# Performance work log

Measured on AMD Instinct MI355X. Metric: run time of the kernel, lower is better.

Reference implementation:

```python
import jax, jax.numpy as jnp
import numpy as np

C, B, N, D, H, DV = 8, 32, 256, 128, 4, 64  # channels, graphs, nodes/graph, gcn_h_dim, heads, d_kv
EPS = 1e-6


def _layernorm(x, g, b):
    mu = jnp.mean(x, axis=-1, keepdims=True)
    var = jnp.mean(jnp.square(x - mu), axis=-1, keepdims=True)
    return (x - mu) * jax.lax.rsqrt(var + EPS) * g + b


def setup_inputs() -> dict:
    key = jax.random.key(0)
    ks = jax.random.split(key, 6)
    gnn_out = jax.random.normal(ks[0], (C, B * N, D), dtype=jnp.float32)
    batch = jnp.repeat(jnp.arange(B, dtype=jnp.int64), N)  # sorted node->graph ids
    s = 0.05  # small init scale keeps softmax well-conditioned
    Wq = jax.random.normal(ks[1], (D, H * DV), dtype=jnp.float32) * s
    Wk = jax.random.normal(ks[2], (D, H * DV), dtype=jnp.float32) * s
    Wv = jax.random.normal(ks[3], (D, H * DV), dtype=jnp.float32) * s
    Wfc = jax.random.normal(ks[4], (H * DV, DV), dtype=jnp.float32) * s
    return {
        "gnn_out": gnn_out,
        "Wq": Wq, "Wk": Wk, "Wv": Wv, "Wfc": Wfc,
        "ln1_g": jnp.ones((DV,), jnp.float32), "ln1_b": jnp.zeros((DV,), jnp.float32),
        "ln2_g": jnp.ones((DV,), jnp.float32), "ln2_b": jnp.zeros((DV,), jnp.float32),
        "batch": batch,
        "sz_b": B,
    }


def reference(gnn_out, Wq, Wk, Wv, Wfc, ln1_g, ln1_b, ln2_g, ln2_b, batch, sz_b):
    sz_c, total, d_model = gnn_out.shape
    nb = sz_b                      # static number of graphs
    n = total // nb                # nodes per graph (equal-sized graphs)
    dv = Wfc.shape[1]
    nh = Wq.shape[1] // dv

    # to_dense_batch for all channels at once: scatter nodes into [B, N, C, D]
    starts = jnp.searchsorted(batch, jnp.arange(nb))
    pos = jnp.arange(total) - starts[batch]
    dense = jnp.zeros((nb, n, sz_c, d_model), gnn_out.dtype)
    dense = dense.at[batch, pos].set(jnp.transpose(gnn_out, (1, 0, 2)))
    x = jnp.transpose(dense, (2, 0, 1, 3)).reshape(sz_c * nb, n, d_model)  # fold channel into batch

    # multi-head projections -> [CB, H, N, dv]
    q = (x @ Wq).reshape(sz_c * nb, n, nh, dv).transpose(0, 2, 1, 3)
    k = (x @ Wk).reshape(sz_c * nb, n, nh, dv).transpose(0, 2, 1, 3)
    v = (x @ Wv).reshape(sz_c * nb, n, nh, dv).transpose(0, 2, 1, 3)

    temp = dv ** 0.5
    attn = jax.nn.softmax(jnp.einsum('bhqd,bhkd->bhqk', q / temp, k), axis=-1)
    # non-standard: out = V^T @ attn @ V  -> [CB, H, dv, dv]
    out = jnp.einsum('bhnd,bhnm->bhdm', v, attn)
    out = jnp.einsum('bhdm,bhme->bhde', out, v)

    out = out.transpose(0, 2, 1, 3).reshape(sz_c * nb, dv, nh * dv)  # [CB, dv, H*dv]
    out = _layernorm(out @ Wfc, ln1_g, ln1_b)                        # [CB, dv, dv]

    out = out.reshape(sz_c, nb, dv, dv).transpose(1, 0, 2, 3)        # [B, C, dv, dv]
    return _layernorm(out, ln2_g, ln2_b)
```

## Files before the change

### kernel.cpp

```cpp
#include <hip/hip_runtime.h>

#define NN 256
#define DM 128
#define NH 4
#define LK 72
#define LT 264

typedef __bf16 bf16;
typedef __attribute__((ext_vector_type(8))) __bf16 bf16x8;
typedef __attribute__((ext_vector_type(4))) float f32x4;
typedef __attribute__((ext_vector_type(16))) float f32x16;

static __device__ __forceinline__ unsigned short f2b(float f) {
  return __builtin_bit_cast(unsigned short, (__bf16)f);
}
static __device__ __forceinline__ bf16x8 ldf(const unsigned short* p) {
  return *(const bf16x8*)p;
}
static __device__ __forceinline__ void st4(unsigned short* p, float a, float b, float c, float d) {
  ushort4 v; v.x = f2b(a); v.y = f2b(b); v.z = f2b(c); v.w = f2b(d);
  *(ushort4*)p = v;
}

#define MFMA16(a,b,c) __builtin_amdgcn_mfma_f32_16x16x32_bf16((a),(b),(c),0,0,0)
#define MFMA32(a,b,c) __builtin_amdgcn_mfma_f32_32x32x16_bf16((a),(b),(c),0,0,0)
#define Z4  {0.f,0.f,0.f,0.f}
#define Z16 {0.f,0.f,0.f,0.f,0.f,0.f,0.f,0.f,0.f,0.f,0.f,0.f,0.f,0.f,0.f,0.f}

#define XELEMS (256u * 16u * 256u * 8u)
#define WQO 0
#define WKO 32768
#define WVO 65536
#define WFO 98304

__global__ void prep_x_kernel(const float* __restrict__ gnn, unsigned short* __restrict__ x2) {
  const int tid = blockIdx.x * 256 + threadIdx.x;
  const int cb  = tid >> 10;
  const int r   = tid & 1023;
  const int dgq = r >> 8;
  const int n   = r & 255;
  const float* src = gnn + ((size_t)cb * 256 + n) * 128;
  unsigned short* dstb = x2 + (size_t)cb * (16 * 256 * 8);
#pragma unroll
  for (int i = 0; i < 4; ++i) {
    const int dg = dgq * 4 + i;
    float4 a = *(const float4*)(src + dg * 8);
    float4 b = *(const float4*)(src + dg * 8 + 4);
    ushort4 u0, u1;
    u0.x = f2b(a.x); u0.y = f2b(a.y); u0.z = f2b(a.z); u0.w = f2b(a.w);
    u1.x = f2b(b.x); u1.y = f2b(b.y); u1.z = f2b(b.z); u1.w = f2b(b.w);
    ushort4* d = (ushort4*)(dstb + ((size_t)dg * 256 + n) * 8);
    d[0] = u0; d[1] = u1;
  }
}

__global__ void prep_w_kernel(const float* __restrict__ Wq, const float* __restrict__ Wk,
                              const float* __restrict__ Wv, const float* __restrict__ Wfc,
                              unsigned short* __restrict__ w2) {
  const int tid = blockIdx.x * 256 + threadIdx.x;
  if (tid < 12288) {
    const int wi  = tid >> 12;
    const int r   = tid & 4095;
    const int dg  = r >> 8, col = r & 255;
    const float* W = (wi == 0) ? Wq : ((wi == 1) ? Wk : Wv);
    unsigned short* d = w2 + wi * 32768 + ((size_t)dg * 256 + col) * 8;
#pragma unroll
    for (int j = 0; j < 8; ++j) d[j] = f2b(W[(size_t)(dg * 8 + j) * 256 + col]);
  } else if (tid < 14336) {
    const int r  = tid - 12288;
    const int dg = r >> 6, col = r & 63;
    unsigned short* d = w2 + WFO + ((size_t)dg * 64 + col) * 8;
#pragma unroll
    for (int j = 0; j < 8; ++j) d[j] = f2b(Wfc[(size_t)(dg * 8 + j) * 64 + col]);
  }
}

template<bool WS>
__global__ __launch_bounds__(512, 2)
void vlrgat_kernel(const float* __restrict__ gnn,
                   const float* __restrict__ Wq, const float* __restrict__ Wk,
                   const float* __restrict__ Wv, const float* __restrict__ Wfc,
                   const float* __restrict__ ln1g, const float* __restrict__ ln1b,
                   const float* __restrict__ ln2g, const float* __restrict__ ln2b,
                   const unsigned short* __restrict__ wsx,
                   const unsigned short* __restrict__ wsw,
                   float* __restrict__ out)
{
  __shared__ __align__(16) unsigned short ks [NN * LK];
  __shared__ __align__(16) unsigned short qs [NN * LK];
  __shared__ __align__(16) unsigned short vsT[64 * LT];
  __shared__ __align__(16) unsigned short U  [NN * LK];
  __shared__ __align__(16) float sums[NN];

  const int t   = threadIdx.x;
  const int w   = t >> 6;
  const int l   = t & 63;
  const int lr  = l & 15;
  const int lg  = l >> 4;
  const int l31 = l & 31;
  const int lh  = l >> 5;
  const int g   = w & 3;
  const int cb  = blockIdx.x;
  const unsigned short* const xw = WS ? (wsx + (size_t)cb * (16 * 256 * 8)) : nullptr;

  f32x16 oacc[NH];
#pragma unroll
  for (int h = 0; h < NH; ++h) oacc[h] = (f32x16)Z16;

  auto xfrag = [&](int n0, int c) -> bf16x8 {
    if constexpr (WS) {
      return ldf(xw + (((size_t)(c * 2 + lh)) * 256 + n0 + l31) * 8);
    } else {
      const float* p = gnn + ((size_t)cb * 256 + n0 + l31) * 128 + c * 16 + lh * 8;
      bf16x8 r;
#pragma unroll
      for (int j = 0; j < 8; ++j) r[j] = (bf16)p[j];
      return r;
    }
  };
  auto wfrag = [&](int wo, const float* __restrict__ W, int c, int col) -> bf16x8 {
    if constexpr (WS) {
      return ldf(wsw + wo + (((size_t)(c * 2 + lh)) * 256 + col) * 8);
    } else {
      bf16x8 r;
#pragma unroll
      for (int j = 0; j < 8; ++j) r[j] = (bf16)W[(size_t)(c * 16 + lh * 8 + j) * 256 + col];
      return r;
    }
  };
  auto wfcfrag = [&](int kt, int col) -> bf16x8 {
    if constexpr (WS) {
      return ldf(wsw + WFO + (((size_t)(kt * 4 + lg)) * 64 + col) * 8);
    } else {
      bf16x8 r;
#pragma unroll
      for (int j = 0; j < 8; ++j) r[j] = (bf16)Wfc[(size_t)(kt * 32 + lg * 8 + j) * 64 + col];
      return r;
    }
  };

#pragma unroll
  for (int h = 0; h < NH; ++h) {
    const float* const WAp = (w < 4) ? Wk : Wv;
    const int       woA    = (w < 4) ? WKO : WVO;
    bf16x8 wA[2][8], wQ[8];
#pragma unroll
    for (int e = 0; e < 2; ++e)
#pragma unroll
      for (int c = 0; c < 8; ++c)
        wA[e][c] = wfrag(woA, WAp, c, h * 64 + e * 32 + l31);
    const int qcol = h * 64 + ((w < 4) ? 0 : 32) + l31;
#pragma unroll
    for (int c = 0; c < 8; ++c)
      wQ[c] = wfrag(WQO, Wq, c, qcol);

    __syncthreads();

#pragma unroll
    for (int half = 0; half < 2; ++half) {
      const int n0 = half * 128 + g * 32;
      bf16x8 xa[8];
#pragma unroll
      for (int c = 0; c < 8; ++c) xa[c] = xfrag(n0, c);
      if (w < 4) {
#pragma unroll
        for (int e = 0; e < 2; ++e) {
          f32x16 a = Z16;
#pragma unroll
          for (int c = 0; c < 8; ++c) a = MFMA32(wA[e][c], xa[c], a);
#pragma unroll
          for (int g2 = 0; g2 < 4; ++g2)
            st4(&ks[(n0 + l31) * LK + e * 32 + g2 * 8 + lh * 4],
                a[g2*4], a[g2*4+1], a[g2*4+2], a[g2*4+3]);
        }
        f32x16 a = Z16;
#pragma unroll
        for (int c = 0; c < 8; ++c) a = MFMA32(wQ[c], xa[c], a);
#pragma unroll
        for (int g2 = 0; g2 < 4; ++g2)
          st4(&qs[(n0 + l31) * LK + g2 * 8 + lh * 4],
              a[g2*4]*0.125f, a[g2*4+1]*0.125f, a[g2*4+2]*0.125f, a[g2*4+3]*0.125f);
      } else {
#pragma unroll
        for (int e = 0; e < 2; ++e) {
          f32x16 a = Z16;
#pragma unroll
          for (int c = 0; c < 8; ++c) a = MFMA32(xa[c], wA[e][c], a);
#pragma unroll
          for (int g2 = 0; g2 < 4; ++g2)
            st4(&vsT[(e * 32 + l31) * LT + n0 + g2 * 8 + lh * 4],
                a[g2*4], a[g2*4+1], a[g2*4+2], a[g2*4+3]);
        }
        f32x16 a = Z16;
#pragma unroll
        for (int c = 0; c < 8; ++c) a = MFMA32(wQ[c], xa[c], a);
#pragma unroll
        for (int g2 = 0; g2 < 4; ++g2)
          st4(&qs[(n0 + l31) * LK + 32 + g2 * 8 + lh * 4],
              a[g2*4]*0.125f, a[g2*4+1]*0.125f, a[g2*4+2]*0.125f, a[g2*4+3]*0.125f);
      }
    }
    __syncthreads();

    bf16x8 qf[4];
#pragma unroll
    for (int kt = 0; kt < 4; ++kt)
      qf[kt] = ldf(&qs[(w * 32 + l31) * LK + kt * 16 + lh * 8]);
    unsigned short* const Pw = &U[(w * 32) * LK];
    f32x16 racc[2]; racc[0] = (f32x16)Z16; racc[1] = (f32x16)Z16;
    float psum = 0.f;
#pragma unroll
    for (int kh = 0; kh < 2; ++kh) {
      f32x16 sh[4];
#pragma unroll
      for (int mb = 0; mb < 4; ++mb) {
        sh[mb] = (f32x16)Z16;
#pragma unroll
        for (int kt = 0; kt < 4; ++kt)
          sh[mb] = MFMA32(ldf(&ks[((kh * 4 + mb) * 32 + l31) * LK + kt * 16 + lh * 8]),
                          qf[kt], sh[mb]);
      }
#pragma unroll
      for (int mb = 0; mb < 4; ++mb)
#pragma unroll
        for (int i = 0; i < 16; ++i) {
          sh[mb][i] = __expf(sh[mb][i]);
          psum += sh[mb][i];
        }
#pragma unroll
      for (int sl = 0; sl < 2; ++sl) {
#pragma unroll
        for (int mbl = 0; mbl < 2; ++mbl) {
          const f32x16& s = sh[sl * 2 + mbl];
#pragma unroll
          for (int g2 = 0; g2 < 4; ++g2)
            st4(&Pw[l31 * LK + mbl * 32 + g2 * 8 + lh * 4],
                s[g2*4], s[g2*4+1], s[g2*4+2], s[g2*4+3]);
        }
        const int kb = kh * 128 + sl * 64;
#pragma unroll
        for (int kt2 = 0; kt2 < 4; ++kt2) {
          bf16x8 pf = ldf(&Pw[l31 * LK + kt2 * 16 + lh * 8]);
          racc[0] = MFMA32(pf, ldf(&vsT[l31 * LT + kb + kt2 * 16 + lh * 8]), racc[0]);
          racc[1] = MFMA32(pf, ldf(&vsT[(32 + l31) * LT + kb + kt2 * 16 + lh * 8]), racc[1]);
        }
      }
    }
    psum += __shfl_xor(psum, 32);
    sums[w * 32 + l31] = psum;

    __syncthreads();

#pragma unroll
    for (int g2 = 0; g2 < 4; ++g2) {
      float4 sv = *(const float4*)&sums[w * 32 + g2 * 8 + lh * 4];
      const float i0 = 1.f / sv.x, i1 = 1.f / sv.y, i2 = 1.f / sv.z, i3 = 1.f / sv.w;
#pragma unroll
      for (int eb = 0; eb < 2; ++eb)
        st4(&U[(eb * 32 + l31) * LT + w * 32 + g2 * 8 + lh * 4],
            racc[eb][g2*4]*i0, racc[eb][g2*4+1]*i1, racc[eb][g2*4+2]*i2, racc[eb][g2*4+3]*i3);
    }
    __syncthreads();

    if (w < 4) {
      const int db = (w >> 1) * 32, eb = (w & 1) * 32;
#pragma unroll
      for (int kt = 0; kt < 16; ++kt)
        oacc[h] = MFMA32(ldf(&vsT[(db + l31) * LT + kt * 16 + lh * 8]),
                         ldf(&U  [(eb + l31) * LT + kt * 16 + lh * 8]), oacc[h]);
    }
  }

  __syncthreads();
  if (w < 4) {
    const int db = (w >> 1) * 32, eb = (w & 1) * 32;
#pragma unroll
    for (int h2 = 0; h2 < NH; ++h2)
#pragma unroll
      for (int g2 = 0; g2 < 4; ++g2)
#pragma unroll
        for (int r = 0; r < 4; ++r)
          U[(db + g2 * 8 + lh * 4 + r) * LT + h2 * 64 + eb + l31] = f2b(oacc[h2][g2*4+r]);
  }
  __syncthreads();

  if (w < 4) {
    bf16x8 oa[8];
#pragma unroll
    for (int kt = 0; kt < 8; ++kt)
      oa[kt] = ldf(&U[(w * 16 + lr) * LT + kt * 32 + lg * 8]);
    f32x4 fa[4];
#pragma unroll
    for (int ct = 0; ct < 4; ++ct) {
      f32x4 a = Z4;
#pragma unroll
      for (int kt = 0; kt < 8; ++kt)
        a = MFMA16(oa[kt], wfcfrag(kt, ct * 16 + lr), a);
      fa[ct] = a;
    }

    float g1v[4], b1v[4], g2v[4], b2v[4];
#pragma unroll
    for (int ct = 0; ct < 4; ++ct) {
      g1v[ct] = ln1g[ct * 16 + lr];
      b1v[ct] = ln1b[ct * 16 + lr];
      g2v[ct] = ln2g[ct * 16 + lr];
      b2v[ct] = ln2b[ct * 16 + lr];
    }
    const int bb = cb & 31;
    const int ch = cb >> 5;
    float* const obase = out + (size_t)(bb * 8 + ch) * 64 * 64;
#pragma unroll
    for (int r = 0; r < 4; ++r) {
      const int row = w * 16 + lg * 4 + r;
      float x0 = fa[0][r], x1 = fa[1][r], x2 = fa[2][r], x3 = fa[3][r];
      float mu = x0 + x1 + x2 + x3;
      mu += __shfl_xor(mu, 1); mu += __shfl_xor(mu, 2);
      mu += __shfl_xor(mu, 4); mu += __shfl_xor(mu, 8);
      mu *= 0.015625f;
      float d0 = x0 - mu, d1 = x1 - mu, d2 = x2 - mu, d3 = x3 - mu;
      float vr = d0*d0 + d1*d1 + d2*d2 + d3*d3;
      vr += __shfl_xor(vr, 1); vr += __shfl_xor(vr, 2);
      vr += __shfl_xor(vr, 4); vr += __shfl_xor(vr, 8);
      const float is1 = rsqrtf(vr * 0.015625f + 1e-6f);
      float y0 = d0*is1*g1v[0] + b1v[0];
      float y1 = d1*is1*g1v[1] + b1v[1];
      float y2 = d2*is1*g1v[2] + b1v[2];
      float y3 = d3*is1*g1v[3] + b1v[3];
      float mu2 = y0 + y1 + y2 + y3;
      mu2 += __shfl_xor(mu2, 1); mu2 += __shfl_xor(mu2, 2);
      mu2 += __shfl_xor(mu2, 4); mu2 += __shfl_xor(mu2, 8);
      mu2 *= 0.015625f;
      float e0 = y0-mu2, e1 = y1-mu2, e2 = y2-mu2, e3 = y3-mu2;
      float v2 = e0*e0 + e1*e1 + e2*e2 + e3*e3;
      v2 += __shfl_xor(v2, 1); v2 += __shfl_xor(v2, 2);
      v2 += __shfl_xor(v2, 4); v2 += __shfl_xor(v2, 8);
      const float is2 = rsqrtf(v2 * 0.015625f + 1e-6f);
      float* const op = obase + (size_t)row * 64;
      op[ 0 + lr] = e0*is2*g2v[0] + b2v[0];
      op[16 + lr] = e1*is2*g2v[1] + b2v[1];
      op[32 + lr] = e2*is2*g2v[2] + b2v[2];
      op[48 + lr] = e3*is2*g2v[3] + b2v[3];
    }
  }
}

extern "C" void kernel_launch(void* const* d_in, const int* in_sizes, int n_in,
                              void* d_out, int out_size, void* d_ws, size_t ws_size,
                              hipStream_t stream) {
  const float* gnn = (const float*)d_in[0];
  const float* Wq  = (const float*)d_in[1];
  const float* Wk  = (const float*)d_in[2];
  const float* Wv  = (const float*)d_in[3];
  const float* Wfc = (const float*)d_in[4];
  const float* l1g = (const float*)d_in[5];
  const float* l1b = (const float*)d_in[6];
  const float* l2g = (const float*)d_in[7];
  const float* l2b = (const float*)d_in[8];
  (void)in_sizes; (void)n_in; (void)out_size;

  const size_t need = ((size_t)XELEMS + 3 * 32768 + 16384) * sizeof(unsigned short);
  unsigned short* wsx = (unsigned short*)d_ws;
  unsigned short* wsw = wsx + XELEMS;

  if (d_ws != nullptr && ws_size >= need) {
    prep_x_kernel<<<dim3(1024), dim3(256), 0, stream>>>(gnn, wsx);
    prep_w_kernel<<<dim3(56), dim3(256), 0, stream>>>(Wq, Wk, Wv, Wfc, wsw);
    vlrgat_kernel<true><<<dim3(256), dim3(512), 0, stream>>>(
        gnn, Wq, Wk, Wv, Wfc, l1g, l1b, l2g, l2b, wsx, wsw, (float*)d_out);
  } else {
    vlrgat_kernel<false><<<dim3(256), dim3(512), 0, stream>>>(
        gnn, Wq, Wk, Wv, Wfc, l1g, l1b, l2g, l2b, nullptr, nullptr, (float*)d_out);
  }
}
```

Baseline: 68.76 us.

## Split attention per (channel-batch, head) into separate blocks and add FC+LayerNorm kernel

The monolithic kernel looped over all four heads in one 256-block grid. It is replaced by a head kernel that launches 1024 blocks, one per (cb, head), with smaller shared memory so four blocks fit per CU. Q now stays in registers as packed bf16 with the 1/sqrt(d) scale folded in. Each head's [64x64] output goes to a workspace buffer, and a separate kernel then does the Wfc projection and both LayerNorms. This trades an extra launch and a global round trip of the head outputs for far more parallelism on a GPU with many CUs.

Measured after the change: 98.80 us. +43.7%, slower.

```diff
diff --git a/kernel.cpp b/kernel.cpp
--- a/kernel.cpp
+++ b/kernel.cpp
@@ -10,6 +10,7 @@
 typedef __attribute__((ext_vector_type(8))) __bf16 bf16x8;
 typedef __attribute__((ext_vector_type(4))) float f32x4;
 typedef __attribute__((ext_vector_type(16))) float f32x16;
+typedef __attribute__((ext_vector_type(4))) unsigned int u32x4;
 
 static __device__ __forceinline__ unsigned short f2b(float f) {
   return __builtin_bit_cast(unsigned short, (__bf16)f);
@@ -20,6 +21,19 @@
 static __device__ __forceinline__ void st4(unsigned short* p, float a, float b, float c, float d) {
   ushort4 v; v.x = f2b(a); v.y = f2b(b); v.z = f2b(c); v.w = f2b(d);
   *(ushort4*)p = v;
+}
+static __device__ __forceinline__ unsigned cvtpk(float lo, float hi) {
+  unsigned r;
+  asm("v_cvt_pk_bf16_f32 %0, %1, %2" : "=v"(r) : "v"(lo), "v"(hi));
+  return r;
+}
+static __device__ __forceinline__ bf16x8 ld2(const unsigned short* p0, const unsigned short* p1) {
+  u32x4 t;
+  t.x = *(const unsigned*)(p0);
+  t.y = *(const unsigned*)(p0 + 2);
+  t.z = *(const unsigned*)(p1);
+  t.w = *(const unsigned*)(p1 + 2);
+  return __builtin_bit_cast(bf16x8, t);
 }
 
 #define MFMA16(a,b,c) __builtin_amdgcn_mfma_f32_16x16x32_bf16((a),(b),(c),0,0,0)
@@ -32,6 +46,8 @@
 #define WKO 32768
 #define WVO 65536
 #define WFO 98304
+#define WELEMS 114688u
+#define OELEMS (256u * 64u * 256u)
 
 __global__ void prep_x_kernel(const float* __restrict__ gnn, unsigned short* __restrict__ x2) {
   const int tid = blockIdx.x * 256 + threadIdx.x;
@@ -75,16 +91,227 @@
   }
 }
 
-template<bool WS>
+__global__ __launch_bounds__(512, 4)
+void vlrgat_head_kernel(const unsigned short* __restrict__ wsx,
+                        const unsigned short* __restrict__ wsw,
+                        unsigned short* __restrict__ wso)
+{
+  __shared__ __align__(16) unsigned short ks [NN * LK];
+  __shared__ __align__(16) unsigned short vsT[64 * LT];
+  __shared__ __align__(16) float sums[NN];
+
+  const int t   = threadIdx.x;
+  const int w   = t >> 6;
+  const int l   = t & 63;
+  const int l31 = l & 31;
+  const int lh  = l >> 5;
+  const int g   = w & 3;
+  const int bid = blockIdx.x;
+  const int cb  = bid >> 2;
+  const int h   = bid & 3;
+  const unsigned short* const xw = wsx + (size_t)cb * (16 * 256 * 8);
+
+  const int woA = (w < 4) ? WKO : WVO;
+  bf16x8 wA[2][8];
+#pragma unroll
+  for (int e = 0; e < 2; ++e)
+#pragma unroll
+    for (int c = 0; c < 8; ++c)
+      wA[e][c] = ldf(wsw + woA + (((size_t)(c * 2 + lh)) * 256 + h * 64 + e * 32 + l31) * 8);
+
+  u32x4 qu[4];
+  const int hw = w >> 2;
+#pragma unroll
+  for (int half = 0; half < 2; ++half) {
+    const int n0 = half * 128 + g * 32;
+    bf16x8 xa[8];
+#pragma unroll
+    for (int c = 0; c < 8; ++c)
+      xa[c] = ldf(xw + (((size_t)(c * 2 + lh)) * 256 + n0 + l31) * 8);
+    if (w < 4) {
+#pragma unroll
+      for (int e = 0; e < 2; ++e) {
+        f32x16 a = Z16;
+#pragma unroll
+        for (int c = 0; c < 8; ++c) a = MFMA32(wA[e][c], xa[c], a);
+#pragma unroll
+        for (int g2 = 0; g2 < 4; ++g2)
+          st4(&ks[(n0 + l31) * LK + e * 32 + g2 * 8 + lh * 4],
+              a[g2*4], a[g2*4+1], a[g2*4+2], a[g2*4+3]);
+      }
+    } else {
+#pragma unroll
+      for (int e = 0; e < 2; ++e) {
+        f32x16 a = Z16;
+#pragma unroll
+        for (int c = 0; c < 8; ++c) a = MFMA32(xa[c], wA[e][c], a);
+#pragma unroll
+        for (int g2 = 0; g2 < 4; ++g2)
+          st4(&vsT[(e * 32 + l31) * LT + n0 + g2 * 8 + lh * 4],
+              a[g2*4], a[g2*4+1], a[g2*4+2], a[g2*4+3]);
+      }
+    }
+    if (half == hw) {
+#pragma unroll
+      for (int e = 0; e < 2; ++e) {
+        bf16x8 wQ[8];
+#pragma unroll
+        for (int c = 0; c < 8; ++c)
+          wQ[c] = ldf(wsw + WQO + (((size_t)(c * 2 + lh)) * 256 + h * 64 + e * 32 + l31) * 8);
+        f32x16 a = Z16;
+#pragma unroll
+        for (int c = 0; c < 8; ++c) a = MFMA32(wQ[c], xa[c], a);
+        const float S = 0.125f;
+        qu[e*2]   = (u32x4){cvtpk(a[0]*S,  a[1]*S),  cvtpk(a[2]*S,  a[3]*S),
+                            cvtpk(a[4]*S,  a[5]*S),  cvtpk(a[6]*S,  a[7]*S)};
+        qu[e*2+1] = (u32x4){cvtpk(a[8]*S,  a[9]*S),  cvtpk(a[10]*S, a[11]*S),
+                            cvtpk(a[12]*S, a[13]*S), cvtpk(a[14]*S, a[15]*S)};
+      }
+    }
+  }
+  __syncthreads();
+
+  f32x16 racc0 = Z16, racc1 = Z16;
+  float psum = 0.f;
+  const int ko1 = 4 * lh, ko2 = 8 + 4 * lh;
+#pragma unroll
+  for (int mb = 0; mb < 8; ++mb) {
+    const unsigned short* krow = &ks[(mb * 32 + l31) * LK];
+    f32x16 s = Z16;
+#pragma unroll
+    for (int kt = 0; kt < 4; ++kt) {
+      bf16x8 kf = ld2(krow + kt * 16 + ko1, krow + kt * 16 + ko2);
+      s = MFMA32(kf, __builtin_bit_cast(bf16x8, qu[kt]), s);
+    }
+#pragma unroll
+    for (int i = 0; i < 16; ++i) { s[i] = __expf(s[i]); psum += s[i]; }
+    u32x4 pu0 = (u32x4){cvtpk(s[0], s[1]),   cvtpk(s[2], s[3]),
+                        cvtpk(s[4], s[5]),   cvtpk(s[6], s[7])};
+    u32x4 pu1 = (u32x4){cvtpk(s[8], s[9]),   cvtpk(s[10], s[11]),
+                        cvtpk(s[12], s[13]), cvtpk(s[14], s[15])};
+#pragma unroll
+    for (int b = 0; b < 2; ++b) {
+      bf16x8 pf = __builtin_bit_cast(bf16x8, b ? pu1 : pu0);
+      const unsigned short* v0 = &vsT[l31 * LT + mb * 32 + b * 16];
+      const unsigned short* v1 = &vsT[(32 + l31) * LT + mb * 32 + b * 16];
+      racc0 = MFMA32(pf, ld2(v0 + ko1, v0 + ko2), racc0);
+      racc1 = MFMA32(pf, ld2(v1 + ko1, v1 + ko2), racc1);
+    }
+  }
+  psum += __shfl_xor(psum, 32);
+  sums[w * 32 + l31] = psum;
+
+  __syncthreads();
+
+  unsigned short* const RsT = ks;
+#pragma unroll
+  for (int g2 = 0; g2 < 4; ++g2) {
+    float4 sv = *(const float4*)&sums[w * 32 + g2 * 8 + lh * 4];
+    const float i0 = 1.f / sv.x, i1 = 1.f / sv.y, i2 = 1.f / sv.z, i3 = 1.f / sv.w;
+    st4(&RsT[l31 * LT + w * 32 + g2 * 8 + lh * 4],
+        racc0[g2*4]*i0, racc0[g2*4+1]*i1, racc0[g2*4+2]*i2, racc0[g2*4+3]*i3);
+    st4(&RsT[(32 + l31) * LT + w * 32 + g2 * 8 + lh * 4],
+        racc1[g2*4]*i0, racc1[g2*4+1]*i1, racc1[g2*4+2]*i2, racc1[g2*4+3]*i3);
+  }
+  __syncthreads();
+
+  if (w < 4) {
+    const int db = (w >> 1) * 32, eb = (w & 1) * 32;
+    f32x16 o = Z16;
+#pragma unroll
+    for (int kt = 0; kt < 16; ++kt)
+      o = MFMA32(ldf(&vsT[(db + l31) * LT + kt * 16 + lh * 8]),
+                 ldf(&RsT[(eb + l31) * LT + kt * 16 + lh * 8]), o);
+    unsigned short* ob = wso + (size_t)cb * 64 * 256;
+#pragma unroll
+    for (int r = 0; r < 16; ++r) {
+      const int d = db + (r & 3) + 8 * (r >> 2) + 4 * lh;
+      ob[(size_t)d * 256 + h * 64 + eb + l31] = f2b(o[r]);
+    }
+  }
+}
+
+__global__ __launch_bounds__(256, 4)
+void fc_ln_kernel(const unsigned short* __restrict__ wso,
+                  const unsigned short* __restrict__ wsw,
+                  const float* __restrict__ ln1g, const float* __restrict__ ln1b,
+                  const float* __restrict__ ln2g, const float* __restrict__ ln2b,
+                  float* __restrict__ out)
+{
+  const int t  = threadIdx.x;
+  const int w  = t >> 6;
+  const int l  = t & 63;
+  const int lr = l & 15;
+  const int lg = l >> 4;
+  const int cb = blockIdx.x;
+  const unsigned short* ob = wso + (size_t)cb * 64 * 256;
+
+  bf16x8 oa[8];
+#pragma unroll
+  for (int kt = 0; kt < 8; ++kt)
+    oa[kt] = ldf(&ob[(w * 16 + lr) * 256 + kt * 32 + lg * 8]);
+  f32x4 fa[4];
+#pragma unroll
+  for (int ct = 0; ct < 4; ++ct) {
+    f32x4 a = Z4;
+#pragma unroll
+    for (int kt = 0; kt < 8; ++kt)
+      a = MFMA16(oa[kt], ldf(wsw + WFO + (((size_t)(kt * 4 + lg)) * 64 + ct * 16 + lr) * 8), a);
+    fa[ct] = a;
+  }
+
+  float g1v[4], b1v[4], g2v[4], b2v[4];
+#pragma unroll
+  for (int ct = 0; ct < 4; ++ct) {
+    g1v[ct] = ln1g[ct * 16 + lr];
+    b1v[ct] = ln1b[ct * 16 + lr];
+    g2v[ct] = ln2g[ct * 16 + lr];
+    b2v[ct] = ln2b[ct * 16 + lr];
+  }
+  const int bb = cb & 31;
+  const int ch = cb >> 5;
+  float* const obase = out + (size_t)(bb * 8 + ch) * 64 * 64;
+#pragma unroll
+  for (int r = 0; r < 4; ++r) {
+    const int row = w * 16 + lg * 4 + r;
+    float x0 = fa[0][r], x1 = fa[1][r], x2 = fa[2][r], x3 = fa[3][r];
+    float mu = x0 + x1 + x2 + x3;
+    mu += __shfl_xor(mu, 1); mu += __shfl_xor(mu, 2);
+    mu += __shfl_xor(mu, 4); mu += __shfl_xor(mu, 8);
+    mu *= 0.015625f;
+    float d0 = x0 - mu, d1 = x1 - mu, d2 = x2 - mu, d3 = x3 - mu;
+    float vr = d0*d0 + d1*d1 + d2*d2 + d3*d3;
+    vr += __shfl_xor(vr, 1); vr += __shfl_xor(vr, 2);
+    vr += __shfl_xor(vr, 4); vr += __shfl_xor(vr, 8);
+    const float is1 = rsqrtf(vr * 0.015625f + 1e-6f);
+    float y0 = d0*is1*g1v[0] + b1v[0];
+    float y1 = d1*is1*g1v[1] + b1v[1];
+    float y2 = d2*is1*g1v[2] + b1v[2];
+    float y3 = d3*is1*g1v[3] + b1v[3];
+    float mu2 = y0 + y1 + y2 + y3;
+    mu2 += __shfl_xor(mu2, 1); mu2 += __shfl_xor(mu2, 2);
+    mu2 += __shfl_xor(mu2, 4); mu2 += __shfl_xor(mu2, 8);
+    mu2 *= 0.015625f;
+    float e0 = y0-mu2, e1 = y1-mu2, e2 = y2-mu2, e3 = y3-mu2;
+    float v2 = e0*e0 + e1*e1 + e2*e2 + e3*e3;
+    v2 += __shfl_xor(v2, 1); v2 += __shfl_xor(v2, 2);
+    v2 += __shfl_xor(v2, 4); v2 += __shfl_xor(v2, 8);
+    const float is2 = rsqrtf(v2 * 0.015625f + 1e-6f);
+    float* const op = obase + (size_t)row * 64;
+    op[ 0 + lr] = e0*is2*g2v[0] + b2v[0];
+    op[16 + lr] = e1*is2*g2v[1] + b2v[1];
+    op[32 + lr] = e2*is2*g2v[2] + b2v[2];
+    op[48 + lr] = e3*is2*g2v[3] + b2v[3];
+  }
+}
+
 __global__ __launch_bounds__(512, 2)
-void vlrgat_kernel(const float* __restrict__ gnn,
-                   const float* __restrict__ Wq, const float* __restrict__ Wk,
-                   const float* __restrict__ Wv, const float* __restrict__ Wfc,
-                   const float* __restrict__ ln1g, const float* __restrict__ ln1b,
-                   const float* __restrict__ ln2g, const float* __restrict__ ln2b,
-                   const unsigned short* __restrict__ wsx,
-                   const unsigned short* __restrict__ wsw,
-                   float* __restrict__ out)
+void vlrgat_fallback(const float* __restrict__ gnn,
+                     const float* __restrict__ Wq, const float* __restrict__ Wk,
+                     const float* __restrict__ Wv, const float* __restrict__ Wfc,
+                     const float* __restrict__ ln1g, const float* __restrict__ ln1b,
+                     const float* __restrict__ ln2g, const float* __restrict__ ln2b,
+                     float* __restrict__ out)
 {
   __shared__ __align__(16) unsigned short ks [NN * LK];
   __shared__ __align__(16) unsigned short qs [NN * LK];
@@ -101,58 +328,38 @@
   const int lh  = l >> 5;
   const int g   = w & 3;
   const int cb  = blockIdx.x;
-  const unsigned short* const xw = WS ? (wsx + (size_t)cb * (16 * 256 * 8)) : nullptr;
 
   f32x16 oacc[NH];
 #pragma unroll
   for (int h = 0; h < NH; ++h) oacc[h] = (f32x16)Z16;
 
   auto xfrag = [&](int n0, int c) -> bf16x8 {
-    if constexpr (WS) {
-      return ldf(xw + (((size_t)(c * 2 + lh)) * 256 + n0 + l31) * 8);
-    } else {
-      const float* p = gnn + ((size_t)cb * 256 + n0 + l31) * 128 + c * 16 + lh * 8;
-      bf16x8 r;
-#pragma unroll
-      for (int j = 0; j < 8; ++j) r[j] = (bf16)p[j];
-      return r;
-    }
+    const float* p = gnn + ((size_t)cb * 256 + n0 + l31) * 128 + c * 16 + lh * 8;
+    bf16x8 r;
+#pragma unroll
+    for (int j = 0; j < 8; ++j) r[j] = (bf16)p[j];
+    return r;
   };
-  auto wfrag = [&](int wo, const float* __restrict__ W, int c, int col) -> bf16x8 {
-    if constexpr (WS) {
-      return ldf(wsw + wo + (((size_t)(c * 2 + lh)) * 256 + col) * 8);
-    } else {
-      bf16x8 r;
-#pragma unroll
-      for (int j = 0; j < 8; ++j) r[j] = (bf16)W[(size_t)(c * 16 + lh * 8 + j) * 256 + col];
-      return r;
-    }
-  };
-  auto wfcfrag = [&](int kt, int col) -> bf16x8 {
-    if constexpr (WS) {
-      return ldf(wsw + WFO + (((size_t)(kt * 4 + lg)) * 64 + col) * 8);
-    } else {
-      bf16x8 r;
-#pragma unroll
-      for (int j = 0; j < 8; ++j) r[j] = (bf16)Wfc[(size_t)(kt * 32 + lg * 8 + j) * 64 + col];
-      return r;
-    }
+  auto wfrag = [&](const float* __restrict__ W, int c, int col) -> bf16x8 {
+    bf16x8 r;
+#pragma unroll
+    for (int j = 0; j < 8; ++j) r[j] = (bf16)W[(size_t)(c * 16 + lh * 8 + j) * 256 + col];
+    return r;
   };
 
 #pragma unroll
   for (int h = 0; h < NH; ++h) {
     const float* const WAp = (w < 4) ? Wk : Wv;
-    const int       woA    = (w < 4) ? WKO : WVO;
     bf16x8 wA[2][8], wQ[8];
 #pragma unroll
     for (int e = 0; e < 2; ++e)
 #pragma unroll
       for (int c = 0; c < 8; ++c)
-        wA[e][c] = wfrag(woA, WAp, c, h * 64 + e * 32 + l31);
+        wA[e][c] = wfrag(WAp, c, h * 64 + e * 32 + l31);
     const int qcol = h * 64 + ((w < 4) ? 0 : 32) + l31;
 #pragma unroll
     for (int c = 0; c < 8; ++c)
-      wQ[c] = wfrag(WQO, Wq, c, qcol);
+      wQ[c] = wfrag(Wq, c, qcol);
 
     __syncthreads();
 
@@ -294,8 +501,12 @@
     for (int ct = 0; ct < 4; ++ct) {
       f32x4 a = Z4;
 #pragma unroll
-      for (int kt = 0; kt < 8; ++kt)
-        a = MFMA16(oa[kt], wfcfrag(kt, ct * 16 + lr), a);
+      for (int kt = 0; kt < 8; ++kt) {
+        bf16x8 wf;
+#pragma unroll
+        for (int j = 0; j < 8; ++j) wf[j] = (bf16)Wfc[(size_t)(kt * 32 + lg * 8 + j) * 64 + ct * 16 + lr];
+        a = MFMA16(oa[kt], wf, a);
+      }
       fa[ct] = a;
     }
 
@@ -359,17 +570,18 @@
   const float* l2b = (const float*)d_in[8];
   (void)in_sizes; (void)n_in; (void)out_size;
 
-  const size_t need = ((size_t)XELEMS + 3 * 32768 + 16384) * sizeof(unsigned short);
+  const size_t need = ((size_t)XELEMS + WELEMS + OELEMS) * sizeof(unsigned short);
   unsigned short* wsx = (unsigned short*)d_ws;
   unsigned short* wsw = wsx + XELEMS;
+  unsigned short* wso = wsw + WELEMS;
 
   if (d_ws != nullptr && ws_size >= need) {
     prep_x_kernel<<<dim3(1024), dim3(256), 0, stream>>>(gnn, wsx);
     prep_w_kernel<<<dim3(56), dim3(256), 0, stream>>>(Wq, Wk, Wv, Wfc, wsw);
-    vlrgat_kernel<true><<<dim3(256), dim3(512), 0, stream>>>(
-        gnn, Wq, Wk, Wv, Wfc, l1g, l1b, l2g, l2b, wsx, wsw, (float*)d_out);
+    vlrgat_head_kernel<<<dim3(1024), dim3(512), 0, stream>>>(wsx, wsw, wso);
+    fc_ln_kernel<<<dim3(256), dim3(256), 0, stream>>>(wso, wsw, l1g, l1b, l2g, l2b, (float*)d_out);
   } else {
-    vlrgat_kernel<false><<<dim3(256), dim3(512), 0, stream>>>(
-        gnn, Wq, Wk, Wv, Wfc, l1g, l1b, l2g, l2b, nullptr, nullptr, (float*)d_out);
-  }
-}
+    vlrgat_fallback<<<dim3(256), dim3(512), 0, stream>>>(
+        gnn, Wq, Wk, Wv, Wfc, l1g, l1b, l2g, l2b, (float*)d_out);
+  }
+}
```

## Drop x prep kernel; load x once into registers and convert in-kernel

Applied to the files above, without the earlier changes.

Removes the separate prep_x kernel, which converted the whole input to a bf16 tiled workspace. The main kernel now reads fp32 rows with float4 loads once before the head loop and keeps the bf16 fragments in registers for both halves and all four heads, instead of reloading them per head. Launch bounds drop to one block per SM to leave room for the extra registers. This saves a kernel launch and a full write plus reread of x, at the cost of lower occupancy and strided fp32 loads.

Measured after the change: 63.46 us. 1.08x faster.

```diff
diff --git a/kernel.cpp b/kernel.cpp
--- a/kernel.cpp
+++ b/kernel.cpp
@@ -27,32 +27,11 @@
 #define Z4  {0.f,0.f,0.f,0.f}
 #define Z16 {0.f,0.f,0.f,0.f,0.f,0.f,0.f,0.f,0.f,0.f,0.f,0.f,0.f,0.f,0.f,0.f}
 
-#define XELEMS (256u * 16u * 256u * 8u)
 #define WQO 0
 #define WKO 32768
 #define WVO 65536
 #define WFO 98304
-
-__global__ void prep_x_kernel(const float* __restrict__ gnn, unsigned short* __restrict__ x2) {
-  const int tid = blockIdx.x * 256 + threadIdx.x;
-  const int cb  = tid >> 10;
-  const int r   = tid & 1023;
-  const int dgq = r >> 8;
-  const int n   = r & 255;
-  const float* src = gnn + ((size_t)cb * 256 + n) * 128;
-  unsigned short* dstb = x2 + (size_t)cb * (16 * 256 * 8);
-#pragma unroll
-  for (int i = 0; i < 4; ++i) {
-    const int dg = dgq * 4 + i;
-    float4 a = *(const float4*)(src + dg * 8);
-    float4 b = *(const float4*)(src + dg * 8 + 4);
-    ushort4 u0, u1;
-    u0.x = f2b(a.x); u0.y = f2b(a.y); u0.z = f2b(a.z); u0.w = f2b(a.w);
-    u1.x = f2b(b.x); u1.y = f2b(b.y); u1.z = f2b(b.z); u1.w = f2b(b.w);
-    ushort4* d = (ushort4*)(dstb + ((size_t)dg * 256 + n) * 8);
-    d[0] = u0; d[1] = u1;
-  }
-}
+#define WELEMS 114688u
 
 __global__ void prep_w_kernel(const float* __restrict__ Wq, const float* __restrict__ Wk,
                               const float* __restrict__ Wv, const float* __restrict__ Wfc,
@@ -76,13 +55,12 @@
 }
 
 template<bool WS>
-__global__ __launch_bounds__(512, 2)
+__global__ __launch_bounds__(512, 1)
 void vlrgat_kernel(const float* __restrict__ gnn,
                    const float* __restrict__ Wq, const float* __restrict__ Wk,
                    const float* __restrict__ Wv, const float* __restrict__ Wfc,
                    const float* __restrict__ ln1g, const float* __restrict__ ln1b,
                    const float* __restrict__ ln2g, const float* __restrict__ ln2b,
-                   const unsigned short* __restrict__ wsx,
                    const unsigned short* __restrict__ wsw,
                    float* __restrict__ out)
 {
@@ -101,23 +79,11 @@
   const int lh  = l >> 5;
   const int g   = w & 3;
   const int cb  = blockIdx.x;
-  const unsigned short* const xw = WS ? (wsx + (size_t)cb * (16 * 256 * 8)) : nullptr;
 
   f32x16 oacc[NH];
 #pragma unroll
   for (int h = 0; h < NH; ++h) oacc[h] = (f32x16)Z16;
 
-  auto xfrag = [&](int n0, int c) -> bf16x8 {
-    if constexpr (WS) {
-      return ldf(xw + (((size_t)(c * 2 + lh)) * 256 + n0 + l31) * 8);
-    } else {
-      const float* p = gnn + ((size_t)cb * 256 + n0 + l31) * 128 + c * 16 + lh * 8;
-      bf16x8 r;
-#pragma unroll
-      for (int j = 0; j < 8; ++j) r[j] = (bf16)p[j];
-      return r;
-    }
-  };
   auto wfrag = [&](int wo, const float* __restrict__ W, int c, int col) -> bf16x8 {
     if constexpr (WS) {
       return ldf(wsw + wo + (((size_t)(c * 2 + lh)) * 256 + col) * 8);
@@ -139,6 +105,21 @@
     }
   };
 
+  bf16x8 xaH[2][8];
+#pragma unroll
+  for (int half = 0; half < 2; ++half) {
+    const float* prow = gnn + ((size_t)cb * 256 + half * 128 + g * 32 + l31) * 128 + lh * 8;
+#pragma unroll
+    for (int c = 0; c < 8; ++c) {
+      float4 a = *(const float4*)(prow + c * 16);
+      float4 b = *(const float4*)(prow + c * 16 + 4);
+      bf16x8 r;
+      r[0] = (bf16)a.x; r[1] = (bf16)a.y; r[2] = (bf16)a.z; r[3] = (bf16)a.w;
+      r[4] = (bf16)b.x; r[5] = (bf16)b.y; r[6] = (bf16)b.z; r[7] = (bf16)b.w;
+      xaH[half][c] = r;
+    }
+  }
+
 #pragma unroll
   for (int h = 0; h < NH; ++h) {
     const float* const WAp = (w < 4) ? Wk : Wv;
@@ -159,9 +140,7 @@
 #pragma unroll
     for (int half = 0; half < 2; ++half) {
       const int n0 = half * 128 + g * 32;
-      bf16x8 xa[8];
-#pragma unroll
-      for (int c = 0; c < 8; ++c) xa[c] = xfrag(n0, c);
+      const bf16x8* xa = xaH[half];
       if (w < 4) {
 #pragma unroll
         for (int e = 0; e < 2; ++e) {
@@ -359,17 +338,15 @@
   const float* l2b = (const float*)d_in[8];
   (void)in_sizes; (void)n_in; (void)out_size;
 
-  const size_t need = ((size_t)XELEMS + 3 * 32768 + 16384) * sizeof(unsigned short);
-  unsigned short* wsx = (unsigned short*)d_ws;
-  unsigned short* wsw = wsx + XELEMS;
+  const size_t need = (size_t)WELEMS * sizeof(unsigned short);
+  unsigned short* wsw = (unsigned short*)d_ws;
 
   if (d_ws != nullptr && ws_size >= need) {
-    prep_x_kernel<<<dim3(1024), dim3(256), 0, stream>>>(gnn, wsx);
     prep_w_kernel<<<dim3(56), dim3(256), 0, stream>>>(Wq, Wk, Wv, Wfc, wsw);
     vlrgat_kernel<true><<<dim3(256), dim3(512), 0, stream>>>(
-        gnn, Wq, Wk, Wv, Wfc, l1g, l1b, l2g, l2b, wsx, wsw, (float*)d_out);
+        gnn, Wq, Wk, Wv, Wfc, l1g, l1b, l2g, l2b, wsw, (float*)d_out);
   } else {
     vlrgat_kernel<false><<<dim3(256), dim3(512), 0, stream>>>(
-        gnn, Wq, Wk, Wv, Wfc, l1g, l1b, l2g, l2b, nullptr, nullptr, (float*)d_out);
-  }
-}
+        gnn, Wq, Wk, Wv, Wfc, l1g, l1b, l2g, l2b, nullptr, (float*)d_out);
+  }
+}
```
